# Performance work log

Hardware: AMD Instinct MI355X
Metric: run time of the kernel (lower is better)

The kernel has to match this reference:

```python
import jax, jax.numpy as jnp
import numpy as np

N_QUERIES = 4096
N_MEM = 32768
D_FEAT = 8
N_VALS = 4  # discrete feature values in {0..3}


def setup_inputs() -> dict:
    key = jax.random.key(0)
    k1, k2, k3, k4, k5 = jax.random.split(key, 5)
    # Discrete-valued feature vectors (bucket-elimination variable assignments),
    # stored as float32 exactly as torch would (tuple(x[i].tolist()) keys).
    x = jax.random.randint(k1, (N_QUERIES, D_FEAT), 0, N_VALS).astype(jnp.float32)
    mem_keys = jax.random.randint(k2, (N_MEM, D_FEAT), 0, N_VALS).astype(jnp.float32)
    mem_values = jax.random.normal(k3, (N_MEM,), dtype=jnp.float32)
    # nn.Linear(D, 1) fallback
    w = jax.random.normal(k4, (1, D_FEAT), dtype=jnp.float32) * (1.0 / np.sqrt(D_FEAT))
    b = jax.random.normal(k5, (1,), dtype=jnp.float32) * 0.01
    return {"x": x, "mem_keys": mem_keys, "mem_values": mem_values, "w": w, "b": b}


def reference(x, mem_keys, mem_values, w, b):
    # Batched exact-match hash-table lookup with linear fallback.
    # eq: [N, M, D] -> match: [N, M]
    match = jnp.all(x[:, None, :] == mem_keys[None, :, :], axis=-1)
    found = jnp.any(match, axis=1)  # [N]
    # Python dict semantics: later duplicate key insertions overwrite earlier
    # ones, so take the LAST matching memory row.
    M = mem_keys.shape[0]
    last_idx = (M - 1) - jnp.argmax(match[:, ::-1], axis=1)  # [N]
    mem_out = mem_values[last_idx]  # [N]
    lin_out = (x @ w.T + b)[:, 0]  # [N] scalar linear fallback
    out = jnp.where(found, mem_out, lin_out)
    return out[:, None]  # [N, 1], matching .view(-1, 1)
```

## Files before the change

### kernel.cpp

```cpp
#include <hip/hip_runtime.h>

#define NQ 4096
#define NM 32768
#define DF 8
#define TABLE_ENTRIES 65536

__device__ __forceinline__ int encode_row(const float* __restrict__ row) {
    const float4* p = reinterpret_cast<const float4*>(row);
    float4 a = p[0];
    float4 c = p[1];
    return  ((int)a.x)       | (((int)a.y) << 2)  | (((int)a.z) << 4)  | (((int)a.w) << 6)
          | (((int)c.x) << 8) | (((int)c.y) << 10) | (((int)c.z) << 12) | (((int)c.w) << 14);
}

__global__ void build_table_kernel(const float* __restrict__ mem_keys,
                                   int* __restrict__ table) {
    int m = blockIdx.x * blockDim.x + threadIdx.x;
    if (m >= NM) return;
    int code = encode_row(mem_keys + m * DF);
    atomicMax(&table[code], m);
}

__global__ void lookup_kernel(const float* __restrict__ x,
                              const float* __restrict__ mem_values,
                              const float* __restrict__ w,
                              const float* __restrict__ bias,
                              const int* __restrict__ table,
                              float* __restrict__ out) {
    int i = blockIdx.x * blockDim.x + threadIdx.x;
    if (i >= NQ) return;
    const float4* p = reinterpret_cast<const float4*>(x + i * DF);
    float4 a = p[0];
    float4 c = p[1];
    int code = ((int)a.x)        | (((int)a.y) << 2)  | (((int)a.z) << 4)  | (((int)a.w) << 6)
             | (((int)c.x) << 8) | (((int)c.y) << 10) | (((int)c.z) << 12) | (((int)c.w) << 14);
    int idx = table[code];
    float r;
    if (idx >= 0) {
        r = mem_values[idx];
    } else {
        r = bias[0]
          + a.x * w[0] + a.y * w[1] + a.z * w[2] + a.w * w[3]
          + c.x * w[4] + c.y * w[5] + c.z * w[6] + c.w * w[7];
    }
    out[i] = r;
}

extern "C" void kernel_launch(void* const* d_in, const int* in_sizes, int n_in,
                              void* d_out, int out_size, void* d_ws, size_t ws_size,
                              hipStream_t stream) {
    const float* x          = (const float*)d_in[0];
    const float* mem_keys   = (const float*)d_in[1];
    const float* mem_values = (const float*)d_in[2];
    const float* w          = (const float*)d_in[3];
    const float* bias       = (const float*)d_in[4];
    float* out              = (float*)d_out;

    int* table = (int*)d_ws;

    hipMemsetAsync(table, 0xFF, TABLE_ENTRIES * sizeof(int), stream);

    build_table_kernel<<<(NM + 255) / 256, 256, 0, stream>>>(mem_keys, table);
    lookup_kernel<<<(NQ + 255) / 256, 256, 0, stream>>>(x, mem_values, w, bias, table, out);
}
```

Before: 14.21 us.

## Fuse memset, table build and lookup into one cooperative kernel with grid syncs

Replaces the memset plus two kernel launches with a single cooperative kernel of 128 blocks. It clears the table, builds it with atomicMax, then does the lookups, using grid.sync between phases. This removes launch overhead and the inter-kernel gaps. In exchange it pays for two grid-wide barriers and uses fewer threads for the build phase, and cooperative launch carries its own overhead.

```diff
diff --git a/kernel.cpp b/kernel.cpp
--- a/kernel.cpp
+++ b/kernel.cpp
@@ -1,49 +1,59 @@
 #include <hip/hip_runtime.h>
+#include <hip/hip_cooperative_groups.h>
+
+namespace cg = cooperative_groups;
 
 #define NQ 4096
 #define NM 32768
 #define DF 8
 #define TABLE_ENTRIES 65536
+#define BLOCKS 128
+#define THREADS 256
+#define NTHREADS (BLOCKS * THREADS)
 
-__device__ __forceinline__ int encode_row(const float* __restrict__ row) {
-    const float4* p = reinterpret_cast<const float4*>(row);
-    float4 a = p[0];
-    float4 c = p[1];
-    return  ((int)a.x)       | (((int)a.y) << 2)  | (((int)a.z) << 4)  | (((int)a.w) << 6)
+__device__ __forceinline__ int encode8(float4 a, float4 c) {
+    return  ((int)a.x)        | (((int)a.y) << 2)  | (((int)a.z) << 4)  | (((int)a.w) << 6)
           | (((int)c.x) << 8) | (((int)c.y) << 10) | (((int)c.z) << 12) | (((int)c.w) << 14);
 }
 
-__global__ void build_table_kernel(const float* __restrict__ mem_keys,
-                                   int* __restrict__ table) {
-    int m = blockIdx.x * blockDim.x + threadIdx.x;
-    if (m >= NM) return;
-    int code = encode_row(mem_keys + m * DF);
-    atomicMax(&table[code], m);
-}
+__global__ void __launch_bounds__(THREADS, 1)
+memorizer_fused(const float* __restrict__ x,
+                const float* __restrict__ mem_keys,
+                const float* __restrict__ mem_values,
+                const float* __restrict__ w,
+                const float* __restrict__ bias,
+                int* __restrict__ table,
+                float* __restrict__ out) {
+    cg::grid_group grid = cg::this_grid();
+    const int tid = blockIdx.x * blockDim.x + threadIdx.x;
 
-__global__ void lookup_kernel(const float* __restrict__ x,
-                              const float* __restrict__ mem_values,
-                              const float* __restrict__ w,
-                              const float* __restrict__ bias,
-                              const int* __restrict__ table,
-                              float* __restrict__ out) {
-    int i = blockIdx.x * blockDim.x + threadIdx.x;
-    if (i >= NQ) return;
-    const float4* p = reinterpret_cast<const float4*>(x + i * DF);
-    float4 a = p[0];
-    float4 c = p[1];
-    int code = ((int)a.x)        | (((int)a.y) << 2)  | (((int)a.z) << 4)  | (((int)a.w) << 6)
-             | (((int)c.x) << 8) | (((int)c.y) << 10) | (((int)c.z) << 12) | (((int)c.w) << 14);
-    int idx = table[code];
-    float r;
-    if (idx >= 0) {
-        r = mem_values[idx];
-    } else {
-        r = bias[0]
-          + a.x * w[0] + a.y * w[1] + a.z * w[2] + a.w * w[3]
-          + c.x * w[4] + c.y * w[5] + c.z * w[6] + c.w * w[7];
+    #pragma unroll
+    for (int i = tid; i < TABLE_ENTRIES; i += NTHREADS) table[i] = -1;
+
+    grid.sync();
+
+    for (int m = tid; m < NM; m += NTHREADS) {
+        const float4* p = reinterpret_cast<const float4*>(mem_keys + m * DF);
+        float4 a = p[0], c = p[1];
+        atomicMax(&table[encode8(a, c)], m);
     }
-    out[i] = r;
+
+    grid.sync();
+
+    if (tid < NQ) {
+        const float4* p = reinterpret_cast<const float4*>(x + tid * DF);
+        float4 a = p[0], c = p[1];
+        int idx = table[encode8(a, c)];
+        float r;
+        if (idx >= 0) {
+            r = mem_values[idx];
+        } else {
+            r = bias[0]
+              + a.x * w[0] + a.y * w[1] + a.z * w[2] + a.w * w[3]
+              + c.x * w[4] + c.y * w[5] + c.z * w[6] + c.w * w[7];
+        }
+        out[tid] = r;
+    }
 }
 
 extern "C" void kernel_launch(void* const* d_in, const int* in_sizes, int n_in,
@@ -55,11 +65,10 @@
     const float* w          = (const float*)d_in[3];
     const float* bias       = (const float*)d_in[4];
     float* out              = (float*)d_out;
+    int* table              = (int*)d_ws;
 
-    int* table = (int*)d_ws;
-
-    hipMemsetAsync(table, 0xFF, TABLE_ENTRIES * sizeof(int), stream);
-
-    build_table_kernel<<<(NM + 255) / 256, 256, 0, stream>>>(mem_keys, table);
-    lookup_kernel<<<(NQ + 255) / 256, 256, 0, stream>>>(x, mem_values, w, bias, table, out);
+    void* args[] = {(void*)&x, (void*)&mem_keys, (void*)&mem_values,
+                    (void*)&w, (void*)&bias, (void*)&table, (void*)&out};
+    hipLaunchCooperativeKernel(reinterpret_cast<void*>(memorizer_fused),
+                               dim3(BLOCKS), dim3(THREADS), args, 0, stream);
 }
```

Result: slower. 48.61 us (+242.0%).
